# Performance work log

Measured on AMD Instinct MI355X. Metric: run time of the kernel, lower is better.

The kernel has to match this reference:

```python
import jax, jax.numpy as jnp
import numpy as np

B, S, D = 32, 1024, 512
DMAX = 8

def setup_inputs() -> dict:
    key = jax.random.key(0)
    k1, k2 = jax.random.split(key)
    x = jax.random.normal(k1, (B, S, D), dtype=jnp.float32)
    durations = jax.random.randint(k2, (B, S), 0, DMAX).astype(jnp.float32)
    return {"x": x, "durations": durations, "duration_scale": 1}

def reference(x, durations, duration_scale):
    # round + clamp(min=1), as in the torch module
    d = jnp.clip((durations * duration_scale + 0.5).astype(jnp.int32), 1, None)  # (B,S)
    total_lengths = d.sum(axis=1)                      # (B,)
    max_len = int(jnp.max(total_lengths))              # concrete batch max (matches torch .item())
    ends = jnp.cumsum(d, axis=1)                       # (B,S) exclusive-end offsets
    pos = jnp.arange(max_len, dtype=jnp.int32)         # (T,)
    # src index for each output frame: number of cumulative ends <= pos
    idx = jax.vmap(lambda e: jnp.searchsorted(e, pos, side="right"))(ends)  # (B,T)
    idx = jnp.minimum(idx, S - 1)
    gathered = jnp.take_along_axis(x, idx[:, :, None], axis=1)  # (B,T,D)
    mask = pos[None, :] < total_lengths[:, None]                # (B,T)
    out = jnp.where(mask[:, :, None], gathered, jnp.zeros((), x.dtype))
    return out, total_lengths
```

## Files before the change

### kernel.cpp

```cpp
#include <hip/hip_runtime.h>

#define BATCH 32

typedef float f32x4 __attribute__((ext_vector_type(4)));

__global__ void lr_scan_kernel(const float* __restrict__ dur,
                               const unsigned int* __restrict__ scale_raw,
                               float* __restrict__ out_tail,
                               int* __restrict__ totals,
                               int* __restrict__ idxmap,
                               int S, int T) {
    __shared__ int partial[256];
    const int b = blockIdx.x;
    const int tid = threadIdx.x;

    unsigned int u = scale_raw[0];
    float scale = (u < 0x00800000u) ? (float)(int)u : __uint_as_float(u);

    const int PER = S / 256;
    int d[8];
    int lsum = 0;
    const int base = tid * PER;
    for (int k = 0; k < PER; ++k) {
        float f = dur[b * S + base + k];
        int di = (int)(f * scale + 0.5f);
        if (di < 1) di = 1;
        d[k] = di;
        lsum += di;
    }
    partial[tid] = lsum;
    __syncthreads();

    for (int off = 1; off < 256; off <<= 1) {
        int t = (tid >= off) ? partial[tid - off] : 0;
        __syncthreads();
        partial[tid] += t;
        __syncthreads();
    }

    int run = partial[tid] - lsum;
    for (int k = 0; k < PER; ++k) {
        int e = run + d[k];
        for (int j = run; j < e; ++j)
            idxmap[b * T + j] = base + k;
        run = e;
    }

    if (tid == 255) {
        int total = partial[255];
        totals[b] = total;
        out_tail[b] = (float)total;
    }
}

__global__ __launch_bounds__(256) void lr_fill_kernel(
        const f32x4* __restrict__ x4,
        const int* __restrict__ idxmap,
        const int* __restrict__ totals,
        f32x4* __restrict__ out4,
        int S, int T, int d4shift) {
    const int b = blockIdx.y;
    const int D4m1 = (1 << d4shift) - 1;
    const int lane = threadIdx.x & D4m1;
    const int fpb = 256 >> d4shift;
    const int t = blockIdx.x * fpb + (threadIdx.x >> d4shift);
    if (t >= T) return;

    f32x4 v = (f32x4)(0.f, 0.f, 0.f, 0.f);
    if (t < totals[b]) {
        const int s = idxmap[b * T + t];
        v = x4[(((long long)(b * S + s)) << d4shift) + lane];
    }
    __builtin_nontemporal_store(v, &out4[(((long long)(b * T + t)) << d4shift) + lane]);
}

extern "C" void kernel_launch(void* const* d_in, const int* in_sizes, int n_in,
                              void* d_out, int out_size, void* d_ws, size_t ws_size,
                              hipStream_t stream) {
    const float* x = (const float*)d_in[0];
    const float* dur = (const float*)d_in[1];
    const unsigned int* scale = (const unsigned int*)d_in[2];

    const int B = BATCH;
    const int D = in_sizes[0] / in_sizes[1];
    const int S = in_sizes[1] / B;
    const int T = (out_size - B) / (B * D);

    float* out = (float*)d_out;
    float* out_tail = out + (long long)B * T * D;

    int* idxmap = (int*)d_ws;
    int* totals = idxmap + (long long)B * T;

    lr_scan_kernel<<<B, 256, 0, stream>>>(dur, scale, out_tail, totals, idxmap, S, T);

    const int D4 = D / 4;
    int d4shift = 0;
    while ((1 << d4shift) < D4) ++d4shift;
    const int fpb = 256 >> d4shift;
    dim3 grid((T + fpb - 1) / fpb, B);
    lr_fill_kernel<<<grid, 256, 0, stream>>>((const f32x4*)x, idxmap, totals,
                                             (f32x4*)out, S, T, d4shift);
}
```

Baseline: 306.4 us.

## Add XCD-swizzled fill kernel processing multiple frames per thread with source reuse

Adds a templated fill kernel for D=512 in which each thread group handles four consecutive output frames. It reuses the loaded source row when consecutive frames map to the same source index, which is common because durations repeat a frame. It also remaps the flat block index so that each XCD gets a contiguous range of work, aiming for better L2 locality on MI355X. The trade-off is fewer blocks, more registers per thread, and a per-frame branch; other D values keep the old kernel.

```diff
diff --git a/kernel.cpp b/kernel.cpp
--- a/kernel.cpp
+++ b/kernel.cpp
@@ -53,6 +53,56 @@
     }
 }
 
+template<int D4SHIFT, int NT>
+__global__ __launch_bounds__(256) void lr_fill_swz_kernel(
+        const f32x4* __restrict__ x4,
+        const int* __restrict__ idxmap,
+        const int* __restrict__ totals,
+        f32x4* __restrict__ out4,
+        int S, int T, int nbx, int nwg) {
+    constexpr int GPB = 256 >> D4SHIFT;
+    constexpr int FPB = GPB * NT;
+
+    const int wg = blockIdx.x;
+    const int q = nwg >> 3, r = nwg & 7;
+    const int xcd = wg & 7, seq = wg >> 3;
+    const int swz = (xcd < r ? xcd * (q + 1) : r * (q + 1) + (xcd - r) * q) + seq;
+
+    const int b  = swz / nbx;
+    const int tb = swz - b * nbx;
+    const int lane = threadIdx.x & ((1 << D4SHIFT) - 1);
+    const int grp  = threadIdx.x >> D4SHIFT;
+    const int t0 = tb * FPB + grp * NT;
+    const int total = totals[b];
+
+    int sarr[NT];
+#pragma unroll
+    for (int k = 0; k < NT; ++k) {
+        const int t = t0 + k;
+        sarr[k] = (t < total) ? idxmap[b * T + t] : -1;
+    }
+
+    const long long xbase = ((long long)b * S) << D4SHIFT;
+    const long long obase = (((long long)b * T + t0) << D4SHIFT) + lane;
+
+    int s_prev = -1;
+    f32x4 v = (f32x4)(0.f, 0.f, 0.f, 0.f);
+#pragma unroll
+    for (int k = 0; k < NT; ++k) {
+        const int t = t0 + k;
+        if (t >= T) break;
+        f32x4 w = (f32x4)(0.f, 0.f, 0.f, 0.f);
+        if (sarr[k] >= 0) {
+            if (sarr[k] != s_prev) {
+                v = x4[xbase + ((long long)sarr[k] << D4SHIFT) + lane];
+                s_prev = sarr[k];
+            }
+            w = v;
+        }
+        __builtin_nontemporal_store(w, &out4[obase + ((long long)k << D4SHIFT)]);
+    }
+}
+
 __global__ __launch_bounds__(256) void lr_fill_kernel(
         const f32x4* __restrict__ x4,
         const int* __restrict__ idxmap,
@@ -95,10 +145,19 @@
     lr_scan_kernel<<<B, 256, 0, stream>>>(dur, scale, out_tail, totals, idxmap, S, T);
 
     const int D4 = D / 4;
-    int d4shift = 0;
-    while ((1 << d4shift) < D4) ++d4shift;
-    const int fpb = 256 >> d4shift;
-    dim3 grid((T + fpb - 1) / fpb, B);
-    lr_fill_kernel<<<grid, 256, 0, stream>>>((const f32x4*)x, idxmap, totals,
-                                             (f32x4*)out, S, T, d4shift);
+    if (D4 == 128) {
+        constexpr int NT = 4;
+        const int FPB = (256 >> 7) * NT;
+        const int nbx = (T + FPB - 1) / FPB;
+        const int nwg = B * nbx;
+        lr_fill_swz_kernel<7, NT><<<nwg, 256, 0, stream>>>(
+            (const f32x4*)x, idxmap, totals, (f32x4*)out, S, T, nbx, nwg);
+    } else {
+        int d4shift = 0;
+        while ((1 << d4shift) < D4) ++d4shift;
+        const int fpb = 256 >> d4shift;
+        dim3 grid((T + fpb - 1) / fpb, B);
+        lr_fill_kernel<<<grid, 256, 0, stream>>>((const f32x4*)x, idxmap, totals,
+                                                 (f32x4*)out, S, T, d4shift);
+    }
 }
```

Measured after the change: 306.2 us. No clear change (-0.1%).
